# Performance work log

Hardware: AMD Instinct MI355X
Metric: run time of the kernel (lower is better)

Reference implementation:

```python
import jax, jax.numpy as jnp
import numpy as np

B, T, I, H, C = 512, 1024, 64, 128, 10


def setup_inputs() -> dict:
    key = jax.random.key(0)
    ks = jax.random.split(key, 12)
    s_in = 1.0 / np.sqrt(I + H)
    s_fc = 1.0 / np.sqrt(H)
    inp = {
        "x": jax.random.normal(ks[0], (B, T, I), dtype=jnp.float32),
        "Wf": jax.random.uniform(ks[1], (H, I + H), jnp.float32, -s_in, s_in),
        "bf": jax.random.uniform(ks[2], (H,), jnp.float32, -s_in, s_in),
        "Wo": jax.random.uniform(ks[3], (H, I + H), jnp.float32, -s_in, s_in),
        "bo": jax.random.uniform(ks[4], (H,), jnp.float32, -s_in, s_in),
        "Wi": jax.random.uniform(ks[5], (H, I + H), jnp.float32, -s_in, s_in),
        "bi": jax.random.uniform(ks[6], (H,), jnp.float32, -s_in, s_in),
        "Wg": jax.random.uniform(ks[7], (H, I + H), jnp.float32, -s_in, s_in),
        "bg": jax.random.uniform(ks[8], (H,), jnp.float32, -s_in, s_in),
        "Wfc": jax.random.uniform(ks[9], (C, H), jnp.float32, -s_fc, s_fc),
        "bfc": jax.random.uniform(ks[10], (C,), jnp.float32, -s_fc, s_fc),
    }
    return inp


def reference(x, Wf, bf, Wo, bo, Wi, bi, Wg, bg, Wfc, bfc):
    # Fuse the 4 gate linears into one GEMM per step: [4H, I+H]
    Wall = jnp.concatenate([Wf, Wo, Wi, Wg], axis=0)      # [4H, I+H]
    ball = jnp.concatenate([bf, bo, bi, bg], axis=0)      # [4H]
    Hd = Wf.shape[0]

    def step(carry, xt):
        h, c = carry                                      # [B,H] each
        combined = jnp.concatenate([xt, h], axis=1)       # [B, I+H]
        gates = combined @ Wall.T + ball                  # [B, 4H]
        f = jax.nn.sigmoid(gates[:, 0 * Hd:1 * Hd])
        o = jax.nn.sigmoid(gates[:, 1 * Hd:2 * Hd])
        i = jax.nn.sigmoid(gates[:, 2 * Hd:3 * Hd])
        g = jnp.tanh(gates[:, 3 * Hd:4 * Hd])
        c = c * f + g * i
        h = c * o  # NOTE: original module multiplies c (no tanh) by o
        return (h, c), None

    b = x.shape[0]
    h0 = jnp.zeros((b, Hd), dtype=x.dtype)
    c0 = jnp.zeros((b, Hd), dtype=x.dtype)
    xs = jnp.swapaxes(x, 0, 1)                            # [T, B, I]
    (h, _), _ = jax.lax.scan(step, (h0, c0), xs)
    return h @ Wfc.T + bfc                                # [B, C]
```

## Files before the change

kernel.cpp:

```cpp
#include <hip/hip_runtime.h>
#include <hip/hip_fp16.h>


typedef _Float16 f16x8 __attribute__((ext_vector_type(8)));
typedef __fp16   hf2   __attribute__((ext_vector_type(2)));
typedef float    f32x4 __attribute__((ext_vector_type(4)));

constexpr int Bc   = 16;
constexpr int Tn   = 1024;
constexpr int In   = 64;
constexpr int Hn   = 128;
constexpr int Cn   = 10;
constexpr int Kn   = 192;
constexpr int ROWB = Kn * 2;
constexpr int BUFB = Bc * ROWB;

__device__ __forceinline__ int swz(int row, int byteInRow) {
    return row * ROWB + (byteInRow ^ ((row & 7) << 4));
}

__global__ __launch_bounds__(512, 2)
void lstm_persist(const float* __restrict__ x,
                  const float* __restrict__ Wf, const float* __restrict__ bf,
                  const float* __restrict__ Wo, const float* __restrict__ bo,
                  const float* __restrict__ Wi, const float* __restrict__ bi,
                  const float* __restrict__ Wg, const float* __restrict__ bg,
                  const float* __restrict__ Wfc, const float* __restrict__ bfc,
                  float* __restrict__ out)
{
    __shared__ __align__(16) char comb[2 * BUFB];
    __shared__ float h32[Bc][Hn];

    const int tid  = threadIdx.x;
    const int lane = tid & 63;
    const int wv   = tid >> 6;
    const int l15  = lane & 15;
    const int lg   = lane >> 4;
    const int b0   = blockIdx.x * Bc;
    const int jh0  = wv * 16;

    const float* Wptr[4] = {Wf, Wo, Wi, Wg};
    const float* bptr[4] = {bf, bo, bi, bg};
    f16x8 wfrag[4][6];
    float bias[4];
#pragma unroll
    for (int gt = 0; gt < 4; ++gt) {
        const float* W = Wptr[gt];
        const int jrow = jh0 + l15;
#pragma unroll
        for (int kt = 0; kt < 6; ++kt) {
            const int base = jrow * Kn + kt * 32 + lg * 8;
            const float4 w0 = *reinterpret_cast<const float4*>(&W[base]);
            const float4 w1 = *reinterpret_cast<const float4*>(&W[base + 4]);
            f16x8 h;
            h[0] = (_Float16)w0.x; h[1] = (_Float16)w0.y;
            h[2] = (_Float16)w0.z; h[3] = (_Float16)w0.w;
            h[4] = (_Float16)w1.x; h[5] = (_Float16)w1.y;
            h[6] = (_Float16)w1.z; h[7] = (_Float16)w1.w;
            wfrag[gt][kt] = h;
        }
        bias[gt] = bptr[gt][jrow];
    }

    const int xrow = tid >> 5;
    const int xi0  = (tid & 31) * 2;
    int addrA[2][6], addrH[2][4], addrX[2];
#pragma unroll
    for (int kt = 0; kt < 6; ++kt) {
        const int o = swz(l15, (kt * 32 + lg * 8) * 2);
        addrA[0][kt] = o; addrA[1][kt] = BUFB + o;
    }
#pragma unroll
    for (int r = 0; r < 4; ++r) {
        const int o = swz(lg * 4 + r, (In + jh0 + l15) * 2);
        addrH[0][r] = o; addrH[1][r] = BUFB + o;
    }
    {
        const int o = swz(xrow, xi0 * 2);
        addrX[0] = o; addrX[1] = BUFB + o;
    }

    float c[4]    = {0.f, 0.f, 0.f, 0.f};
    float hreg[4] = {0.f, 0.f, 0.f, 0.f};
    {
        for (int o = tid * 8; o < BUFB; o += 512 * 8)
            *reinterpret_cast<unsigned long long*>(comb + o) = 0ull;
    }
    __syncthreads();
    {
        const float2 xv = *reinterpret_cast<const float2*>(
            &x[((size_t)(b0 + xrow) * Tn + 0) * In + xi0]);
        *reinterpret_cast<hf2*>(comb + addrX[0]) =
            __builtin_amdgcn_cvt_pkrtz(xv.x, xv.y);
    }

    const float* xbase = &x[(size_t)(b0 + xrow) * Tn * In + xi0];
    float2 xv0 = *reinterpret_cast<const float2*>(&xbase[(size_t)1 * In]);
    float2 xv1 = *reinterpret_cast<const float2*>(&xbase[(size_t)2 * In]);

    __syncthreads();

#define LSTM_STEP(P, T)                                                        \
    {                                                                          \
                    \
        *reinterpret_cast<hf2*>(comb + addrX[(P) ^ 1]) =                       \
            __builtin_amdgcn_cvt_pkrtz(xv0.x, xv0.y);                          \
        xv0 = xv1;                                                             \
        {                                                                      \
            const int tf = ((T) + 3 < Tn) ? (T) + 3 : (Tn - 1);                \
            xv1 = *reinterpret_cast<const float2*>(&xbase[(size_t)tf * In]);   \
        }                                                                      \
        f16x8 a[6];                                                            \
        _Pragma("unroll")                                                      \
        for (int kt = 0; kt < 6; ++kt)                                         \
            a[kt] = *reinterpret_cast<const f16x8*>(comb + addrA[P][kt]);      \
        f32x4 acc[4];                                                          \
        _Pragma("unroll")                                                      \
        for (int gt = 0; gt < 4; ++gt) {                                       \
            const float bb = bias[gt];                                         \
            acc[gt] = (f32x4){bb, bb, bb, bb};                                 \
        }                                                                      \
        _Pragma("unroll")                                                      \
        for (int kt = 0; kt < 6; ++kt)                                         \
            _Pragma("unroll")                                                  \
            for (int gt = 0; gt < 4; ++gt)                                     \
                acc[gt] = __builtin_amdgcn_mfma_f32_16x16x32_f16(              \
                    a[kt], wfrag[gt][kt], acc[gt], 0, 0, 0);                   \
                                       \
        _Pragma("unroll")                                                      \
        for (int r = 0; r < 4; ++r) {                                          \
            const float fg = __builtin_amdgcn_rcpf(1.f + __expf(-acc[0][r]));  \
            const float og = __builtin_amdgcn_rcpf(1.f + __expf(-acc[1][r]));  \
            const float ig = __builtin_amdgcn_rcpf(1.f + __expf(-acc[2][r]));  \
            const float gg = fmaf(                                             \
                -2.f, __builtin_amdgcn_rcpf(1.f + __expf(2.f * acc[3][r])),    \
                1.f);                                                          \
            c[r]    = fmaf(c[r], fg, ig * gg);                                 \
            hreg[r] = c[r] * og;                                               \
            *reinterpret_cast<_Float16*>(comb + addrH[(P) ^ 1][r]) =           \
                (_Float16)hreg[r];                                             \
        }                                                                      \
        __syncthreads();                                                       \
    }

    for (int t = 0; t < Tn; t += 2) {
        LSTM_STEP(0, t)
        LSTM_STEP(1, t + 1)
    }
#undef LSTM_STEP

#pragma unroll
    for (int r = 0; r < 4; ++r)
        h32[lg * 4 + r][jh0 + l15] = hreg[r];
    __syncthreads();

    if (tid < Bc * Cn) {
        const int row = tid / Cn;
        const int cc  = tid % Cn;
        float a2 = bfc[cc];
#pragma unroll 4
        for (int jh = 0; jh < Hn; ++jh)
            a2 += h32[row][jh] * Wfc[cc * Hn + jh];
        out[(size_t)(b0 + row) * Cn + cc] = a2;
    }
}

extern "C" void kernel_launch(void* const* d_in, const int* in_sizes, int n_in,
                              void* d_out, int out_size, void* d_ws, size_t ws_size,
                              hipStream_t stream) {
    const float* xp  = (const float*)d_in[0];
    const float* Wfp = (const float*)d_in[1];
    const float* bfp = (const float*)d_in[2];
    const float* Wop = (const float*)d_in[3];
    const float* bop = (const float*)d_in[4];
    const float* Wip = (const float*)d_in[5];
    const float* bip = (const float*)d_in[6];
    const float* Wgp = (const float*)d_in[7];
    const float* bgp = (const float*)d_in[8];
    const float* Wfc = (const float*)d_in[9];
    const float* bfc = (const float*)d_in[10];
    float* outp = (float*)d_out;

    lstm_persist<<<512 / Bc, 512, 0, stream>>>(xp, Wfp, bfp, Wop, bop, Wip, bip,
                                               Wgp, bgp, Wfc, bfc, outp);
}
```

Baseline: 942.3 us.

## Halve waves per block, give each wave two hidden tiles, prescale weights for exp2

Each block now runs 4 waves instead of 8. Each wave owns 32 hidden units (two 16-wide MFMA tiles), reuses the A fragments across both tiles, and loads x as float4. Gate weights and biases are prescaled by log2(e) (doubled for the tanh gate), which lets the activations use raw exp2 instead of expf. This is meant to cut the per-step barrier cost and LDS A-fragment reads. In exchange each wave carries twice the MFMA work and register pressure on the serial critical path.

```diff
diff --git a/kernel.cpp b/kernel.cpp
--- a/kernel.cpp
+++ b/kernel.cpp
@@ -3,6 +3,7 @@
 
 
 typedef _Float16 f16x8 __attribute__((ext_vector_type(8)));
+typedef _Float16 f16x4 __attribute__((ext_vector_type(4)));
 typedef __fp16   hf2   __attribute__((ext_vector_type(2)));
 typedef float    f32x4 __attribute__((ext_vector_type(4)));
 
@@ -19,7 +20,7 @@
     return row * ROWB + (byteInRow ^ ((row & 7) << 4));
 }
 
-__global__ __launch_bounds__(512, 2)
+__global__ __launch_bounds__(256, 1)
 void lstm_persist(const float* __restrict__ x,
                   const float* __restrict__ Wf, const float* __restrict__ bf,
                   const float* __restrict__ Wo, const float* __restrict__ bo,
@@ -37,109 +38,138 @@
     const int l15  = lane & 15;
     const int lg   = lane >> 4;
     const int b0   = blockIdx.x * Bc;
-    const int jh0  = wv * 16;
+    const int jh0  = wv * 32;
 
     const float* Wptr[4] = {Wf, Wo, Wi, Wg};
     const float* bptr[4] = {bf, bo, bi, bg};
-    f16x8 wfrag[4][6];
-    float bias[4];
+    f16x8 wfrag[4][6][2];
+    float bias[4][2];
 #pragma unroll
     for (int gt = 0; gt < 4; ++gt) {
         const float* W = Wptr[gt];
-        const int jrow = jh0 + l15;
-#pragma unroll
-        for (int kt = 0; kt < 6; ++kt) {
-            const int base = jrow * Kn + kt * 32 + lg * 8;
-            const float4 w0 = *reinterpret_cast<const float4*>(&W[base]);
-            const float4 w1 = *reinterpret_cast<const float4*>(&W[base + 4]);
-            f16x8 h;
-            h[0] = (_Float16)w0.x; h[1] = (_Float16)w0.y;
-            h[2] = (_Float16)w0.z; h[3] = (_Float16)w0.w;
-            h[4] = (_Float16)w1.x; h[5] = (_Float16)w1.y;
-            h[6] = (_Float16)w1.z; h[7] = (_Float16)w1.w;
-            wfrag[gt][kt] = h;
+        const float s = (gt == 3) ? 2.8853900817779268f : 1.4426950408889634f;
+#pragma unroll
+        for (int jt = 0; jt < 2; ++jt) {
+            const int jrow = jh0 + jt * 16 + l15;
+#pragma unroll
+            for (int kt = 0; kt < 6; ++kt) {
+                const int base = jrow * Kn + kt * 32 + lg * 8;
+                const float4 w0 = *reinterpret_cast<const float4*>(&W[base]);
+                const float4 w1 = *reinterpret_cast<const float4*>(&W[base + 4]);
+                f16x8 h;
+                h[0] = (_Float16)(w0.x * s); h[1] = (_Float16)(w0.y * s);
+                h[2] = (_Float16)(w0.z * s); h[3] = (_Float16)(w0.w * s);
+                h[4] = (_Float16)(w1.x * s); h[5] = (_Float16)(w1.y * s);
+                h[6] = (_Float16)(w1.z * s); h[7] = (_Float16)(w1.w * s);
+                wfrag[gt][kt][jt] = h;
+            }
+            bias[gt][jt] = bptr[gt][jrow] * s;
         }
-        bias[gt] = bptr[gt][jrow];
-    }
-
-    const int xrow = tid >> 5;
-    const int xi0  = (tid & 31) * 2;
-    int addrA[2][6], addrH[2][4], addrX[2];
+    }
+
+    const int xrow = tid >> 4;
+    const int xi0  = (tid & 15) * 4;
+    int addrA[2][6], addrH[2][8], addrX[2];
 #pragma unroll
     for (int kt = 0; kt < 6; ++kt) {
         const int o = swz(l15, (kt * 32 + lg * 8) * 2);
         addrA[0][kt] = o; addrA[1][kt] = BUFB + o;
     }
 #pragma unroll
-    for (int r = 0; r < 4; ++r) {
-        const int o = swz(lg * 4 + r, (In + jh0 + l15) * 2);
-        addrH[0][r] = o; addrH[1][r] = BUFB + o;
-    }
+    for (int jt = 0; jt < 2; ++jt)
+#pragma unroll
+        for (int r = 0; r < 4; ++r) {
+            const int o = swz(lg * 4 + r, (In + jh0 + jt * 16 + l15) * 2);
+            addrH[0][jt * 4 + r] = o; addrH[1][jt * 4 + r] = BUFB + o;
+        }
     {
         const int o = swz(xrow, xi0 * 2);
         addrX[0] = o; addrX[1] = BUFB + o;
     }
 
-    float c[4]    = {0.f, 0.f, 0.f, 0.f};
-    float hreg[4] = {0.f, 0.f, 0.f, 0.f};
+    float c[2][4], hreg[2][4];
+#pragma unroll
+    for (int jt = 0; jt < 2; ++jt)
+#pragma unroll
+        for (int r = 0; r < 4; ++r) { c[jt][r] = 0.f; hreg[jt][r] = 0.f; }
     {
-        for (int o = tid * 8; o < BUFB; o += 512 * 8)
+        for (int o = tid * 8; o < BUFB; o += 256 * 8)
             *reinterpret_cast<unsigned long long*>(comb + o) = 0ull;
     }
     __syncthreads();
     {
-        const float2 xv = *reinterpret_cast<const float2*>(
+        const float4 xv = *reinterpret_cast<const float4*>(
             &x[((size_t)(b0 + xrow) * Tn + 0) * In + xi0]);
-        *reinterpret_cast<hf2*>(comb + addrX[0]) =
-            __builtin_amdgcn_cvt_pkrtz(xv.x, xv.y);
+        const hf2 p0 = __builtin_amdgcn_cvt_pkrtz(xv.x, xv.y);
+        const hf2 p1 = __builtin_amdgcn_cvt_pkrtz(xv.z, xv.w);
+        f16x4 pk;
+        pk[0] = (_Float16)p0[0]; pk[1] = (_Float16)p0[1];
+        pk[2] = (_Float16)p1[0]; pk[3] = (_Float16)p1[1];
+        *reinterpret_cast<f16x4*>(comb + addrX[0]) = pk;
     }
 
     const float* xbase = &x[(size_t)(b0 + xrow) * Tn * In + xi0];
-    float2 xv0 = *reinterpret_cast<const float2*>(&xbase[(size_t)1 * In]);
-    float2 xv1 = *reinterpret_cast<const float2*>(&xbase[(size_t)2 * In]);
+    float4 xv0 = *reinterpret_cast<const float4*>(&xbase[(size_t)1 * In]);
+    float4 xv1 = *reinterpret_cast<const float4*>(&xbase[(size_t)2 * In]);
 
     __syncthreads();
 
 #define LSTM_STEP(P, T)                                                        \
     {                                                                          \
                     \
-        *reinterpret_cast<hf2*>(comb + addrX[(P) ^ 1]) =                       \
-            __builtin_amdgcn_cvt_pkrtz(xv0.x, xv0.y);                          \
+        {                                                                      \
+            const hf2 p0 = __builtin_amdgcn_cvt_pkrtz(xv0.x, xv0.y);           \
+            const hf2 p1 = __builtin_amdgcn_cvt_pkrtz(xv0.z, xv0.w);           \
+            f16x4 pk;                                                          \
+            pk[0] = (_Float16)p0[0]; pk[1] = (_Float16)p0[1];                  \
+            pk[2] = (_Float16)p1[0]; pk[3] = (_Float16)p1[1];                  \
+            *reinterpret_cast<f16x4*>(comb + addrX[(P) ^ 1]) = pk;             \
+        }                                                                      \
         xv0 = xv1;                                                             \
         {                                                                      \
             const int tf = ((T) + 3 < Tn) ? (T) + 3 : (Tn - 1);                \
-            xv1 = *reinterpret_cast<const float2*>(&xbase[(size_t)tf * In]);   \
+            xv1 = *reinterpret_cast<const float4*>(&xbase[(size_t)tf * In]);   \
         }                                                                      \
         f16x8 a[6];                                                            \
         _Pragma("unroll")                                                      \
         for (int kt = 0; kt < 6; ++kt)                                         \
             a[kt] = *reinterpret_cast<const f16x8*>(comb + addrA[P][kt]);      \
-        f32x4 acc[4];                                                          \
-        _Pragma("unroll")                                                      \
-        for (int gt = 0; gt < 4; ++gt) {                                       \
-            const float bb = bias[gt];                                         \
-            acc[gt] = (f32x4){bb, bb, bb, bb};                                 \
-        }                                                                      \
+        f32x4 acc[4][2];                                                       \
+        _Pragma("unroll")                                                      \
+        for (int gt = 0; gt < 4; ++gt)                                         \
+            _Pragma("unroll")                                                  \
+            for (int jt = 0; jt < 2; ++jt) {                                   \
+                const float bb = bias[gt][jt];                                 \
+                acc[gt][jt] = (f32x4){bb, bb, bb, bb};                         \
+            }                                                                  \
         _Pragma("unroll")                                                      \
         for (int kt = 0; kt < 6; ++kt)                                         \
             _Pragma("unroll")                                                  \
             for (int gt = 0; gt < 4; ++gt)                                     \
-                acc[gt] = __builtin_amdgcn_mfma_f32_16x16x32_f16(              \
-                    a[kt], wfrag[gt][kt], acc[gt], 0, 0, 0);                   \
-                                       \
-        _Pragma("unroll")                                                      \
-        for (int r = 0; r < 4; ++r) {                                          \
-            const float fg = __builtin_amdgcn_rcpf(1.f + __expf(-acc[0][r]));  \
-            const float og = __builtin_amdgcn_rcpf(1.f + __expf(-acc[1][r]));  \
-            const float ig = __builtin_amdgcn_rcpf(1.f + __expf(-acc[2][r]));  \
-            const float gg = fmaf(                                             \
-                -2.f, __builtin_amdgcn_rcpf(1.f + __expf(2.f * acc[3][r])),    \
-                1.f);                                                          \
-            c[r]    = fmaf(c[r], fg, ig * gg);                                 \
-            hreg[r] = c[r] * og;                                               \
-            *reinterpret_cast<_Float16*>(comb + addrH[(P) ^ 1][r]) =           \
-                (_Float16)hreg[r];                                             \
-        }                                                                      \
+                _Pragma("unroll")                                              \
+                for (int jt = 0; jt < 2; ++jt)                                 \
+                    acc[gt][jt] = __builtin_amdgcn_mfma_f32_16x16x32_f16(      \
+                        a[kt], wfrag[gt][kt][jt], acc[gt][jt], 0, 0, 0);       \
+        \
+        _Pragma("unroll")                                                      \
+        for (int jt = 0; jt < 2; ++jt)                                         \
+            _Pragma("unroll")                                                  \
+            for (int r = 0; r < 4; ++r) {                                      \
+                const float fg = __builtin_amdgcn_rcpf(                        \
+                    1.f + __builtin_amdgcn_exp2f(-acc[0][jt][r]));             \
+                const float og = __builtin_amdgcn_rcpf(                        \
+                    1.f + __builtin_amdgcn_exp2f(-acc[1][jt][r]));             \
+                const float ig = __builtin_amdgcn_rcpf(                        \
+                    1.f + __builtin_amdgcn_exp2f(-acc[2][jt][r]));             \
+                const float gg = fmaf(                                         \
+                    -2.f, __builtin_amdgcn_rcpf(                               \
+                              1.f + __builtin_amdgcn_exp2f(acc[3][jt][r])),    \
+                    1.f);                                                      \
+                c[jt][r]    = fmaf(c[jt][r], fg, ig * gg);                     \
+                hreg[jt][r] = c[jt][r] * og;                                   \
+                *reinterpret_cast<_Float16*>(                                  \
+                    comb + addrH[(P) ^ 1][jt * 4 + r]) = (_Float16)hreg[jt][r];\
+            }                                                                  \
         __syncthreads();                                                       \
     }
 
@@ -150,8 +180,10 @@
 #undef LSTM_STEP
 
 #pragma unroll
-    for (int r = 0; r < 4; ++r)
-        h32[lg * 4 + r][jh0 + l15] = hreg[r];
+    for (int jt = 0; jt < 2; ++jt)
+#pragma unroll
+        for (int r = 0; r < 4; ++r)
+            h32[lg * 4 + r][jh0 + jt * 16 + l15] = hreg[jt][r];
     __syncthreads();
 
     if (tid < Bc * Cn) {
@@ -181,6 +213,6 @@
     const float* bfc = (const float*)d_in[10];
     float* outp = (float*)d_out;
 
-    lstm_persist<<<512 / Bc, 512, 0, stream>>>(xp, Wfp, bfp, Wop, bop, Wip, bip,
+    lstm_persist<<<512 / Bc, 256, 0, stream>>>(xp, Wfp, bfp, Wop, bop, Wip, bip,
                                                Wgp, bgp, Wfc, bfc, outp);
 }
```

Result: slower. 1.112 ms (+18.0%).
